# Kernel optimization log

Hardware: AMD Instinct MI355X
Metric: run time of the kernel (lower is better)

## Reference

```python
import jax, jax.numpy as jnp
import numpy as np

WS = 800      # window size
HEADS = 3
DH = 24       # dim_head
LOWRANK_W = 30
NEG_SLOPE = 0.01  # LeakyReLU default
LN_EPS = 1e-5


def _layernorm(x, g, b):
    m = jnp.mean(x, axis=-1, keepdims=True)
    v = jnp.var(x, axis=-1, keepdims=True)
    return (x - m) * jax.lax.rsqrt(v + LN_EPS) * g + b


def setup_inputs() -> dict:
    key = jax.random.key(0)
    ks = jax.random.split(key, 20)
    B, CIN, H, W = 2, 5, 160, 160
    D = 48
    INNER = HEADS * DH  # 72
    f32 = jnp.float32

    def n(k, shape, s=0.05):
        return jax.random.normal(k, shape, f32) * s

    return {
        "x": jax.random.normal(ks[0], (B, CIN, H, W), f32),
        # Embedding: Conv2d(5, 48, 3, pad=1) + PReLU
        "conv_w": n(ks[1], (D, CIN, 3, 3), 0.1),
        "conv_b": jnp.zeros((D,), f32),
        "prelu_a": jnp.array(0.25, f32),
        # attention PreNorm
        "ln1_g": jnp.ones((D,), f32),
        "ln1_b": jnp.zeros((D,), f32),
        # to_qkv: Linear(48, 216, bias=False)
        "w_qkv": n(ks[2], (3 * INNER, D)),
        # Linformer low-rank params E,F: [heads, dim_head, w]
        "E_mat": jax.random.normal(ks[3], (HEADS, DH, LOWRANK_W), f32),
        "F_mat": jax.random.normal(ks[4], (HEADS, DH, LOWRANK_W), f32),
        # lin1/lin2: Linear(w, dim_head)
        "w_e": n(ks[5], (DH, LOWRANK_W)),
        "b_e": jnp.zeros((DH,), f32),
        "w_f": n(ks[6], (DH, LOWRANK_W)),
        "b_f": jnp.zeros((DH,), f32),
        # to_out: Linear(72, 48)
        "w_out": n(ks[7], (D, INNER)),
        "b_out": jnp.zeros((D,), f32),
        # FF PreNorm + MLP (dim=48, hidden=48)
        "ln2_g": jnp.ones((D,), f32),
        "ln2_b": jnp.zeros((D,), f32),
        "ff_w1": n(ks[8], (D, D)),
        "ff_b1": jnp.zeros((D,), f32),
        "ff_w2": n(ks[9], (D, D)),
        "ff_b2": jnp.zeros((D,), f32),
        # final lin1: Linear(48, 96)
        "w_fin": n(ks[10], (2 * D, D)),
        "b_fin": jnp.zeros((2 * D,), f32),
    }


def reference(x, conv_w, conv_b, prelu_a, ln1_g, ln1_b, w_qkv, E_mat, F_mat,
              w_e, b_e, w_f, b_f, w_out, b_out, ln2_g, ln2_b,
              ff_w1, ff_b1, ff_w2, ff_b2, w_fin, b_fin):
    B, _, H, W = x.shape
    # Embedding: conv3x3 same + PReLU
    E = jax.lax.conv_general_dilated(
        x, conv_w, (1, 1), ((1, 1), (1, 1)),
        dimension_numbers=("NCHW", "OIHW", "NCHW")) + conv_b[None, :, None, None]
    E = jnp.maximum(E, 0) + prelu_a * jnp.minimum(E, 0)
    D = E.shape[1]
    seq = E.reshape(B, D, H * W).transpose(0, 2, 1)  # [B, N, D]
    N = seq.shape[1]
    nw = N // WS

    # --- Residual(PreNorm(LinformerAttention_wind1)) ---
    xn = _layernorm(seq, ln1_g, ln1_b)
    xw = xn.reshape(B, nw, WS, D)                         # windows
    qkv = jnp.einsum("bwnc,oc->bwno", xw, w_qkv)          # [B,nw,WS,216]
    qkv = qkv.reshape(B, nw, WS, HEADS, 3 * DH).transpose(0, 1, 3, 2, 4)
    q, k, v = jnp.split(qkv, 3, axis=-1)                  # each [B,nw,h,WS,DH]
    # einsum 'b h n d, h d d -> b h n d' == scale by diagonal of lin(E/F)
    e_diag = jnp.einsum("hdw,dw->hd", E_mat, w_e) + b_e   # [h, DH]
    f_diag = jnp.einsum("hdw,dw->hd", F_mat, w_f) + b_f
    k = k * e_diag[None, None, :, None, :]
    v = v * f_diag[None, None, :, None, :]
    scale = DH ** -0.5
    dots = jnp.einsum("bwhid,bwhjd->bwhij", q, k) * scale  # [B,nw,h,WS,WS]
    attn = jax.nn.softmax(dots, axis=-1)
    ow = jnp.einsum("bwhij,bwhjd->bwhid", attn, v)
    ow = ow.transpose(0, 1, 3, 2, 4).reshape(B, N, HEADS * DH)
    att = jnp.einsum("bnf,of->bno", ow, w_out) + b_out
    seq = seq + att

    # --- Residual(PreNorm(FeedForward)) ---
    yn = _layernorm(seq, ln2_g, ln2_b)
    h = jnp.einsum("bnc,oc->bno", yn, ff_w1) + ff_b1
    h = jnp.where(h >= 0, h, NEG_SLOPE * h)
    h = jnp.einsum("bno,co->bnc", h, ff_w2) + ff_b2
    att1 = seq + h                                        # [B, N, D]

    hp = att1.transpose(0, 2, 1).reshape(B, D, H, W)
    Highpass1 = E * hp + E
    lin = jnp.einsum("bnc,oc->bno", att1, w_fin) + b_fin  # [B, N, 2D]
    return (Highpass1, lin)
```

## Files before the change

kernel.cpp:

```cpp
#include <hip/hip_runtime.h>
#include <hip/hip_bf16.h>

#define B_    2
#define CIN_  5
#define H_    160
#define W_    160
#define N_    25600
#define D_    48
#define NW_   32
#define WS_   800
#define HEADS_ 3
#define DH_   24
#define INNER_ 72
#define NWH_  192

typedef __bf16 bf16x8 __attribute__((ext_vector_type(8)));
typedef float  f32x4  __attribute__((ext_vector_type(4)));

#define MFMA(a,b,c) __builtin_amdgcn_mfma_f32_16x16x32_bf16((a),(b),(c),0,0,0)

__device__ __forceinline__ float fast_exp2(float x) {
#if __has_builtin(__builtin_amdgcn_exp2f)
    return __builtin_amdgcn_exp2f(x);
#else
    return exp2f(x);
#endif
}

__device__ __forceinline__ unsigned pack_bf16(float lo, float hi) {
    __bf16 l = (__bf16)lo, h = (__bf16)hi;
    unsigned short ul = __builtin_bit_cast(unsigned short, l);
    unsigned short uh = __builtin_bit_cast(unsigned short, h);
    return ((unsigned)uh << 16) | (unsigned)ul;
}

__global__ __launch_bounds__(256) void k_wprep(const float* __restrict__ wqkv,
                                               const float* __restrict__ w_out,
                                               const float* __restrict__ fw1,
                                               const float* __restrict__ fw2,
                                               const float* __restrict__ wfin,
                                               const float* __restrict__ cw,
                                               const float* __restrict__ Em,
                                               const float* __restrict__ Fm,
                                               const float* __restrict__ we,
                                               const float* __restrict__ be,
                                               const float* __restrict__ wf,
                                               const float* __restrict__ bf,
                                               float* __restrict__ diag,
                                               __bf16* __restrict__ wqB,
                                               __bf16* __restrict__ woB,
                                               __bf16* __restrict__ f1B,
                                               __bf16* __restrict__ f2B,
                                               __bf16* __restrict__ wfB,
                                               __bf16* __restrict__ wcB) {
    if (blockIdx.x == 0 && threadIdx.x < 72) {
        int tt = threadIdx.x;
        int h = tt / 24, d = tt % 24;
        float se = be[d], sf = bf[d];
        for (int w = 0; w < 30; ++w) {
            se += Em[(h*24+d)*30 + w] * we[d*30 + w];
            sf += Fm[(h*24+d)*30 + w] * wf[d*30 + w];
        }
        diag[tt]      = se;
        diag[72 + tt] = sf;
    }
    int t = blockIdx.x*256 + threadIdx.x, stride = gridDim.x*256;
    for (int i = t; i < 288*64; i += stride) {
        int grow = i>>6, c = i&63;
        int gg = grow>>5, q = grow&31, tt = q>>4, sp = q&15, d = tt*16+sp;
        int part = gg/3, head = gg%3;
        wqB[i] = (d<24 && c<48) ? (__bf16)wqkv[(head*72 + part*24 + d)*48 + c] : (__bf16)0.f;
    }
    for (int i = t; i < 48*96;  i += stride) {
        int o = i/96, p = i%96;
        int h = p>>5, q = p&31, j = q&1, sp = q>>1, d = j*16+sp;
        woB[i] = (d<24) ? (__bf16)w_out[o*72 + h*24 + d] : (__bf16)0.f;
    }
    for (int i = t; i < 48*64;  i += stride) { int o=i>>6, c=i&63; f1B[i] = (c<48)? (__bf16)fw1[o*48+c] : (__bf16)0.f; }
    for (int i = t; i < 48*64;  i += stride) { int o=i>>6, c=i&63; f2B[i] = (c<48)? (__bf16)fw2[o*48+c] : (__bf16)0.f; }
    for (int i = t; i < 96*64;  i += stride) { int o=i>>6, c=i&63; wfB[i] = (c<48)? (__bf16)wfin[o*48+c] : (__bf16)0.f; }
    for (int i = t; i < 48*64;  i += stride) { int o=i>>6, c=i&63; wcB[i] = (c<45)? (__bf16)cw[o*45+c] : (__bf16)0.f; }
}

__global__ __launch_bounds__(128) void k_cqkv(const float* __restrict__ x,
                                              const __bf16* __restrict__ wcB,
                                              const float* __restrict__ cb,
                                              const float* __restrict__ pa,
                                              const __bf16* __restrict__ wqB,
                                              const float* __restrict__ g1,
                                              const float* __restrict__ b1,
                                              const float* __restrict__ diag,
                                              float* __restrict__ seqT,
                                              __bf16* __restrict__ Qbf,
                                              __bf16* __restrict__ Kbf,
                                              __bf16* __restrict__ Vt) {
    __shared__ float Lx[CIN_][4][W_];
    __shared__ __bf16 ic2[64*64];
    __shared__ __bf16 xfer[2][2048];
    int t = threadIdx.x;
    int blk = blockIdx.x;
    int b = blk / 400;
    int n0 = (blk % 400) * 64;
    int y0 = n0 / W_;

    for (int i = t; i < CIN_*4*W_; i += 128) {
        int ic = i / (4*W_), rem = i % (4*W_), yy = rem / W_, col = rem % W_;
        int yr = y0 - 1 + yy;
        float v = 0.f;
        if (yr >= 0 && yr < H_)
            v = x[((size_t)(b*CIN_ + ic)*H_ + yr)*W_ + col];
        Lx[ic][yy][col] = v;
    }
    __syncthreads();

    {
        int px = t & 63;
        int hf = t >> 6;
        int n  = n0 + px;
        int y  = n / W_, xx = n % W_;
        int dy = y - y0;
        char* ib = (char*)ic2;
        int sw = (px&7) << 4;
        if (hf == 0) {
            #pragma unroll
            for (int k = 0; k < 32; ++k) {
                int ic = k/9, rem = k%9, ky = rem/3, kx = rem%3;
                int xc = xx + kx - 1;
                float v = (xc >= 0 && xc < W_) ? Lx[ic][dy+ky][xc] : 0.f;
                *(__bf16*)(ib + ((px*128 + k*2) ^ sw)) = (__bf16)v;
            }
        } else {
            #pragma unroll
            for (int j = 0; j < 32; ++j) {
                int k = 32 + j;
                float v = 0.f;
                if (k < 45) {
                    int ic = k/9, rem = k%9, ky = rem/3, kx = rem%3;
                    int xc = xx + kx - 1;
                    v = (xc >= 0 && xc < W_) ? Lx[ic][dy+ky][xc] : 0.f;
                }
                *(__bf16*)(ib + ((px*128 + k*2) ^ sw)) = (__bf16)v;
            }
        }
    }
    __syncthreads();

    int wv = t >> 6, lane = t & 63, g = lane>>4, s = lane&15;
    int grow0 = blk*64 + wv*32;

    bf16x8 ac[2][2];
    {
        char* ib = (char*)ic2;
        #pragma unroll
        for (int m = 0; m < 2; ++m)
          #pragma unroll
          for (int kc = 0; kc < 2; ++kc) {
            int row = wv*32 + m*16 + s;
            ac[m][kc] = *(const bf16x8*)(ib + ((row*128 + kc*64 + g*16) ^ ((row&7)<<4)));
          }
    }
    const bf16x8* WC4 = (const bf16x8*)wcB;
    float a = pa[0];
    float cbv[3];
    #pragma unroll
    for (int n = 0; n < 3; ++n) cbv[n] = cb[n*16+s];

    float xr[2][3][4];
    #pragma unroll
    for (int n = 0; n < 3; ++n) {
        bf16x8 wb0 = WC4[(n*16+s)*8 + g];
        bf16x8 wb1 = WC4[(n*16+s)*8 + 4 + g];
        #pragma unroll
        for (int m = 0; m < 2; ++m) {
            f32x4 c = {0.f,0.f,0.f,0.f};
            c = MFMA(ac[m][0], wb0, c);
            c = MFMA(ac[m][1], wb1, c);
            #pragma unroll
            for (int r = 0; r < 4; ++r) {
                float vv = c[r] + cbv[n];
                vv = vv >= 0.f ? vv : a * vv;
                xr[m][n][r] = vv;
            }
        }
    }
    #pragma unroll
    for (int m = 0; m < 2; ++m)
      #pragma unroll
      for (int n = 0; n < 3; ++n)
        #pragma unroll
        for (int r = 0; r < 4; ++r)
          seqT[(size_t)(grow0 + m*16 + g*4 + r)*48 + n*16 + s] = xr[m][n][r];

    char* xb = (char*)&xfer[wv][0];
    int nrem = grow0 % N_;
    int w = nrem / WS_, i0 = nrem % WS_;
    size_t headbase = (size_t)((b*NW_ + w)*HEADS_);

    float g1v[3], b1v[3];
    #pragma unroll
    for (int n = 0; n < 3; ++n) { g1v[n] = g1[n*16+s]; b1v[n] = b1[n*16+s]; }

    #pragma unroll
    for (int m = 0; m < 2; ++m)
      #pragma unroll
      for (int r = 0; r < 4; ++r) {
        float sm = xr[m][0][r] + xr[m][1][r] + xr[m][2][r];
        float sq = xr[m][0][r]*xr[m][0][r] + xr[m][1][r]*xr[m][1][r] + xr[m][2][r]*xr[m][2][r];
        #pragma unroll
        for (int msk = 1; msk < 16; msk <<= 1) { sm += __shfl_xor(sm, msk); sq += __shfl_xor(sq, msk); }
        float mean = sm * (1.f/48.f);
        float var  = sq * (1.f/48.f) - mean*mean;
        float rs   = rsqrtf(var + 1e-5f);
        int row = m*16 + g*4 + r;
        int sw  = ((g*4+r)&7) << 4;
        #pragma unroll
        for (int n = 0; n < 3; ++n) {
            float yn = (xr[m][n][r] - mean) * rs * g1v[n] + b1v[n];
            *(__bf16*)(xb + ((row*128 + (n*16+s)*2) ^ sw)) = (__bf16)yn;
        }
        *(__bf16*)(xb + ((row*128 + (48+s)*2) ^ sw)) = (__bf16)0.f;
      }

    bf16x8 af[2][2];
    #pragma unroll
    for (int m = 0; m < 2; ++m)
      #pragma unroll
      for (int kc = 0; kc < 2; ++kc)
        af[m][kc] = *(const bf16x8*)(xb + (((m*16+s)*128 + kc*64 + g*16) ^ ((s&7)<<4)));

    const bf16x8* WQ4 = (const bf16x8*)wqB;
    const float SCALE = 0.2944889919f;

    float dke[3], dko[3], dve[3], dvo[3];
    #pragma unroll
    for (int h = 0; h < 3; ++h) {
        dke[h] = diag[h*24 + s];
        dko[h] = (s < 8) ? diag[h*24 + 16 + s] : 0.f;
        dve[h] = diag[72 + h*24 + s];
        dvo[h] = (s < 8) ? diag[72 + h*24 + 16 + s] : 0.f;
    }

    unsigned* Qd = (unsigned*)Qbf;
    unsigned* Kd = (unsigned*)Kbf;

    #pragma unroll
    for (int gg = 0; gg < 9; ++gg) {
        int part = gg / 3, head = gg % 3;
        bf16x8 we0 = WQ4[(gg*32 +      s)*8 +     g];
        bf16x8 we1 = WQ4[(gg*32 +      s)*8 + 4 + g];
        bf16x8 wo0 = WQ4[(gg*32 + 16 + s)*8 +     g];
        bf16x8 wo1 = WQ4[(gg*32 + 16 + s)*8 + 4 + g];
        f32x4 ce[2], co[2];
        #pragma unroll
        for (int m = 0; m < 2; ++m) {
            f32x4 c = {0.f,0.f,0.f,0.f};
            c = MFMA(af[m][0], we0, c); c = MFMA(af[m][1], we1, c);
            ce[m] = c;
            f32x4 d = {0.f,0.f,0.f,0.f};
            d = MFMA(af[m][0], wo0, d); d = MFMA(af[m][1], wo1, d);
            co[m] = d;
        }
        size_t rbase = (headbase + head)*WS_ + i0;
        if (part == 0) {
            #pragma unroll
            for (int m = 0; m < 2; ++m)
              #pragma unroll
              for (int r = 0; r < 4; ++r)
                Qd[(rbase + m*16 + g*4 + r)*16 + s] =
                    pack_bf16(ce[m][r]*SCALE, co[m][r]*SCALE);
        } else if (part == 1) {
            #pragma unroll
            for (int m = 0; m < 2; ++m)
              #pragma unroll
              for (int r = 0; r < 4; ++r) {
                int p5 = 16*(g&1) + 8*m + 4*(g>>1) + r;
                Kd[(rbase + p5)*16 + s] =
                    pack_bf16(ce[m][r]*dke[head], co[m][r]*dko[head]);
              }
        } else {
            size_t vbase = (headbase + head)*((size_t)32*WS_) + i0;
            #pragma unroll
            for (int m = 0; m < 2; ++m)
              #pragma unroll
              for (int r = 0; r < 4; ++r) {
                int row = m*16 + g*4 + r;
                Vt[vbase + (size_t)s*WS_ + row] = (__bf16)(ce[m][r]*dve[head]);
                if (s < 8)
                    Vt[vbase + (size_t)(16+s)*WS_ + row] = (__bf16)(co[m][r]*dvo[head]);
              }
        }
    }
    unsigned* Vd = (unsigned*)Vt;
    #pragma unroll
    for (int it = 0; it < 6; ++it) {
        int idx = it*64 + lane;
        int h = idx >> 7, rem = idx & 127;
        int dd = 24 + (rem >> 4), cp = rem & 15;
        size_t ubase = (((headbase + h)*((size_t)32*WS_) + (size_t)dd*WS_ + i0) >> 1);
        Vd[ubase + cp] = (dd == 24) ? 0x3F803F80u : 0u;
    }
}

__global__ __launch_bounds__(256, 4) void k_attn(const __bf16* __restrict__ Qbf,
                                                 const __bf16* __restrict__ Kbf,
                                                 const __bf16* __restrict__ Vt,
                                                 __bf16* __restrict__ OW) {
    __shared__ float red[2][5][2][4][64];
    int t = threadIdx.x;
    int wv = t >> 6, lane = t & 63;
    int g = lane >> 4, s = lane & 15;
    int half = wv & 1, tsk = wv >> 1;
    int blk = blockIdx.x;
    int v = (blk & 7) * 120 + (blk >> 3);
    int task = v * 2 + tsk;
    int wh = task / 10, qt = task % 10;
    int q0 = qt * 80;

    const bf16x8* Qp = (const bf16x8*)(Qbf + ((size_t)wh*WS_ + q0)*32);
    const bf16x8* Kp = (const bf16x8*)(Kbf + (size_t)wh*WS_*32);
    const bf16x8* Vp = (const bf16x8*)(Vt  + (size_t)wh*32*WS_);

    bf16x8 qb[5];
    #pragma unroll
    for (int i = 0; i < 5; ++i) qb[i] = Qp[(i*16 + s)*4 + g];

    f32x4 o[5][2];
    #pragma unroll
    for (int i = 0; i < 5; ++i) {
        o[i][0] = (f32x4){0.f,0.f,0.f,0.f};
        o[i][1] = (f32x4){0.f,0.f,0.f,0.f};
    }

    int c0 = half ? 12 : 0;
    int c1 = half ? 25 : 12;

    bf16x8 ka0 = Kp[(c0*32 + s)*4 + g];
    bf16x8 ka1 = Kp[(c0*32 + 16 + s)*4 + g];
    bf16x8 vb0 = Vp[s*100 + c0*4 + g];
    bf16x8 vb1 = Vp[(16+s)*100 + c0*4 + g];

    for (int c = c0; c < c1; ++c) {
        int cn = (c + 1 < c1) ? c + 1 : c0;
        bf16x8 nk0 = Kp[(cn*32 + s)*4 + g];
        bf16x8 nk1 = Kp[(cn*32 + 16 + s)*4 + g];
        bf16x8 nv0 = Vp[s*100 + cn*4 + g];
        bf16x8 nv1 = Vp[(16+s)*100 + cn*4 + g];

        #pragma unroll
        for (int i = 0; i < 5; ++i) {
            f32x4 s0 = {0.f,0.f,0.f,0.f}, s1 = {0.f,0.f,0.f,0.f};
            s0 = MFMA(ka0, qb[i], s0);
            s1 = MFMA(ka1, qb[i], s1);
            bf16x8 pa;
            #pragma unroll
            for (int r = 0; r < 4; ++r) {
                pa[r]     = (__bf16)fast_exp2(s0[r]);
                pa[r + 4] = (__bf16)fast_exp2(s1[r]);
            }
            o[i][0] = MFMA(pa, vb0, o[i][0]);
            o[i][1] = MFMA(pa, vb1, o[i][1]);
        }
        ka0 = nk0; ka1 = nk1; vb0 = nv0; vb1 = nv1;
    }

    if (half) {
        #pragma unroll
        for (int i = 0; i < 5; ++i)
          #pragma unroll
          for (int j = 0; j < 2; ++j)
            #pragma unroll
            for (int r = 0; r < 4; ++r)
              red[tsk][i][j][r][lane] = o[i][j][r];
    }
    __syncthreads();
    if (!half) {
        #pragma unroll
        for (int i = 0; i < 5; ++i)
          #pragma unroll
          for (int j = 0; j < 2; ++j)
            #pragma unroll
            for (int r = 0; r < 4; ++r)
              o[i][j][r] += red[tsk][i][j][r][lane];

        int bw = wh / 3, h = wh % 3;
        int b = bw >> 5, w = bw & 31;
        unsigned* OWd = (unsigned*)OW;
        #pragma unroll
        for (int i = 0; i < 5; ++i) {
            #pragma unroll
            for (int r = 0; r < 4; ++r) {
                float den = __shfl(o[i][1][r], (lane & 48) + 8);
                float inv = 1.f / den;
                int n = w*WS_ + q0 + i*16 + g*4 + r;
                OWd[(size_t)(b*N_ + n)*48 + h*16 + s] =
                    pack_bf16(o[i][0][r]*inv, o[i][1][r]*inv);
            }
        }
    }
}

__global__ __launch_bounds__(256) void k_tail(const float* __restrict__ seqT,
                                              const __bf16* __restrict__ OW,
                                              const __bf16* __restrict__ woB,
                                              const float* __restrict__ b_out,
                                              const float* __restrict__ g2,
                                              const float* __restrict__ b2,
                                              const __bf16* __restrict__ f1B,
                                              const float* __restrict__ fb1,
                                              const __bf16* __restrict__ f2B,
                                              const float* __restrict__ fb2,
                                              const __bf16* __restrict__ wfB,
                                              const float* __restrict__ bfin,
                                              float* __restrict__ out1,
                                              float* __restrict__ out2) {
    __shared__ __bf16 xfer[4][2048];
    __shared__ float hp[4][32][49];
    int t = threadIdx.x, wv = t>>6, lane = t&63, g = lane>>4, s = lane&15;
    int row0 = (blockIdx.x*4 + wv) * 32;
    char* xb = (char*)&xfer[wv][0];

    int b = row0 / N_;
    int nbase = row0 % N_;

    const bf16x8* OW4 = (const bf16x8*)OW;
    const bf16x8* WO4 = (const bf16x8*)woB;
    const bf16x8* F14 = (const bf16x8*)f1B;
    const bf16x8* F24 = (const bf16x8*)f2B;
    const bf16x8* WF4 = (const bf16x8*)wfB;

    bf16x8 aow[2][3];
    #pragma unroll
    for (int m = 0; m < 2; ++m)
      #pragma unroll
      for (int kc = 0; kc < 3; ++kc)
        aow[m][kc] = OW4[(size_t)(row0 + m*16 + s)*12 + kc*4 + g];

    f32x4 s2[2][3];
    #pragma unroll
    for (int n = 0; n < 3; ++n) {
        bf16x8 wb0 = WO4[(n*16+s)*12 + g];
        bf16x8 wb1 = WO4[(n*16+s)*12 + 4 + g];
        bf16x8 wb2 = WO4[(n*16+s)*12 + 8 + g];
        #pragma unroll
        for (int m = 0; m < 2; ++m) {
            f32x4 c = {0.f,0.f,0.f,0.f};
            c = MFMA(aow[m][0], wb0, c);
            c = MFMA(aow[m][1], wb1, c);
            c = MFMA(aow[m][2], wb2, c);
            s2[m][n] = c;
        }
    }
    float bov[3], g2v[3], b2v[3], f1bv[3], f2bv[3];
    #pragma unroll
    for (int n = 0; n < 3; ++n) {
        bov[n] = b_out[n*16+s]; g2v[n] = g2[n*16+s]; b2v[n] = b2[n*16+s];
        f1bv[n] = fb1[n*16+s];  f2bv[n] = fb2[n*16+s];
    }
    float sv[2][3][4];
    #pragma unroll
    for (int m = 0; m < 2; ++m)
      #pragma unroll
      for (int n = 0; n < 3; ++n)
        #pragma unroll
        for (int r = 0; r < 4; ++r) {
          sv[m][n][r] = seqT[(size_t)(row0 + m*16 + g*4 + r)*48 + n*16 + s];
          s2[m][n][r] += sv[m][n][r] + bov[n];
        }

    #pragma unroll
    for (int m = 0; m < 2; ++m)
      #pragma unroll
      for (int r = 0; r < 4; ++r) {
        float sm = s2[m][0][r] + s2[m][1][r] + s2[m][2][r];
        float sq = s2[m][0][r]*s2[m][0][r] + s2[m][1][r]*s2[m][1][r] + s2[m][2][r]*s2[m][2][r];
        #pragma unroll
        for (int msk = 1; msk < 16; msk <<= 1) { sm += __shfl_xor(sm, msk); sq += __shfl_xor(sq, msk); }
        float mean = sm * (1.f/48.f);
        float var  = sq * (1.f/48.f) - mean*mean;
        float rs   = rsqrtf(var + 1e-5f);
        int row = m*16 + g*4 + r;
        int sw  = ((g*4+r)&7) << 4;
        #pragma unroll
        for (int n = 0; n < 3; ++n) {
            float yn = (s2[m][n][r] - mean) * rs * g2v[n] + b2v[n];
            *(__bf16*)(xb + ((row*128 + (n*16+s)*2) ^ sw)) = (__bf16)yn;
        }
        *(__bf16*)(xb + ((row*128 + (48+s)*2) ^ sw)) = (__bf16)0.f;
      }

    bf16x8 af[2][2];
    f32x4 hh[2][3];

    #pragma unroll
    for (int m = 0; m < 2; ++m)
      #pragma unroll
      for (int kc = 0; kc < 2; ++kc)
        af[m][kc] = *(const bf16x8*)(xb + (((m*16+s)*128 + kc*64 + g*16) ^ ((s&7)<<4)));
    #pragma unroll
    for (int n = 0; n < 3; ++n) {
        bf16x8 wb0 = F14[(n*16+s)*8 + g];
        bf16x8 wb1 = F14[(n*16+s)*8 + 4 + g];
        #pragma unroll
        for (int m = 0; m < 2; ++m) {
            f32x4 c = {0.f,0.f,0.f,0.f};
            c = MFMA(af[m][0], wb0, c);
            c = MFMA(af[m][1], wb1, c);
            hh[m][n] = c;
        }
    }
    #pragma unroll
    for (int m = 0; m < 2; ++m)
      #pragma unroll
      for (int r = 0; r < 4; ++r) {
        int row = m*16 + g*4 + r;
        int sw  = ((g*4+r)&7) << 4;
        #pragma unroll
        for (int n = 0; n < 3; ++n) {
            float v = hh[m][n][r] + f1bv[n];
            v = v >= 0.f ? v : 0.01f*v;
            *(__bf16*)(xb + ((row*128 + (n*16+s)*2) ^ sw)) = (__bf16)v;
        }
        *(__bf16*)(xb + ((row*128 + (48+s)*2) ^ sw)) = (__bf16)0.f;
      }

    #pragma unroll
    for (int m = 0; m < 2; ++m)
      #pragma unroll
      for (int kc = 0; kc < 2; ++kc)
        af[m][kc] = *(const bf16x8*)(xb + (((m*16+s)*128 + kc*64 + g*16) ^ ((s&7)<<4)));
    #pragma unroll
    for (int n = 0; n < 3; ++n) {
        bf16x8 wb0 = F24[(n*16+s)*8 + g];
        bf16x8 wb1 = F24[(n*16+s)*8 + 4 + g];
        #pragma unroll
        for (int m = 0; m < 2; ++m) {
            f32x4 c = {0.f,0.f,0.f,0.f};
            c = MFMA(af[m][0], wb0, c);
            c = MFMA(af[m][1], wb1, c);
            hh[m][n] = c;
        }
    }
    #pragma unroll
    for (int m = 0; m < 2; ++m)
      #pragma unroll
      for (int r = 0; r < 4; ++r) {
        int row = m*16 + g*4 + r;
        int sw  = ((g*4+r)&7) << 4;
        #pragma unroll
        for (int n = 0; n < 3; ++n) {
            float a1v = s2[m][n][r] + hh[m][n][r] + f2bv[n];
            hp[wv][row][n*16+s] = sv[m][n][r] * (1.f + a1v);
            *(__bf16*)(xb + ((row*128 + (n*16+s)*2) ^ sw)) = (__bf16)a1v;
        }
        *(__bf16*)(xb + ((row*128 + (48+s)*2) ^ sw)) = (__bf16)0.f;
      }

    #pragma unroll
    for (int it = 0; it < 6; ++it) {
        int flat = it*256 + lane*4;
        int ch = flat >> 5, row = flat & 31;
        float4 v = { hp[wv][row][ch], hp[wv][row+1][ch],
                     hp[wv][row+2][ch], hp[wv][row+3][ch] };
        *(float4*)&out1[((size_t)b*D_ + ch)*N_ + nbase + row] = v;
    }

    #pragma unroll
    for (int m = 0; m < 2; ++m)
      #pragma unroll
      for (int kc = 0; kc < 2; ++kc)
        af[m][kc] = *(const bf16x8*)(xb + (((m*16+s)*128 + kc*64 + g*16) ^ ((s&7)<<4)));
    #pragma unroll
    for (int n = 0; n < 6; ++n) {
        bf16x8 wb0 = WF4[(n*16+s)*8 + g];
        bf16x8 wb1 = WF4[(n*16+s)*8 + 4 + g];
        float bfv = bfin[n*16+s];
        #pragma unroll
        for (int m = 0; m < 2; ++m) {
            f32x4 c = {0.f,0.f,0.f,0.f};
            c = MFMA(af[m][0], wb0, c);
            c = MFMA(af[m][1], wb1, c);
            #pragma unroll
            for (int r = 0; r < 4; ++r)
                out2[(size_t)(row0 + m*16 + g*4 + r)*96 + n*16 + s] = c[r] + bfv;
        }
    }
}

extern "C" void kernel_launch(void* const* d_in, const int* in_sizes, int n_in,
                              void* d_out, int out_size, void* d_ws, size_t ws_size,
                              hipStream_t stream) {
    const float* x      = (const float*)d_in[0];
    const float* conv_w = (const float*)d_in[1];
    const float* conv_b = (const float*)d_in[2];
    const float* prelu_a= (const float*)d_in[3];
    const float* ln1_g  = (const float*)d_in[4];
    const float* ln1_b  = (const float*)d_in[5];
    const float* w_qkv  = (const float*)d_in[6];
    const float* E_mat  = (const float*)d_in[7];
    const float* F_mat  = (const float*)d_in[8];
    const float* w_e    = (const float*)d_in[9];
    const float* b_e    = (const float*)d_in[10];
    const float* w_f    = (const float*)d_in[11];
    const float* b_f    = (const float*)d_in[12];
    const float* w_out  = (const float*)d_in[13];
    const float* b_out  = (const float*)d_in[14];
    const float* ln2_g  = (const float*)d_in[15];
    const float* ln2_b  = (const float*)d_in[16];
    const float* ff_w1  = (const float*)d_in[17];
    const float* ff_b1  = (const float*)d_in[18];
    const float* ff_w2  = (const float*)d_in[19];
    const float* ff_b2  = (const float*)d_in[20];
    const float* w_fin  = (const float*)d_in[21];
    const float* b_fin  = (const float*)d_in[22];

    float* ws = (float*)d_ws;
    float*  seqT = ws;
    float*  diag = seqT + (size_t)B_*N_*D_;
    __bf16* Qbf  = (__bf16*)(diag + 144);
    __bf16* Kbf  = Qbf + (size_t)NWH_*WS_*32;
    __bf16* Vt   = Kbf + (size_t)NWH_*WS_*32;
    __bf16* OW   = Vt + (size_t)NWH_*32*WS_;
    __bf16* wqB  = OW + (size_t)B_*N_*96;
    __bf16* woB  = wqB + 288*64;
    __bf16* f1B  = woB + 48*96;
    __bf16* f2B  = f1B + 48*64;
    __bf16* wfB  = f2B + 48*64;
    __bf16* wcB  = wfB + 96*64;

    float* out1 = (float*)d_out;
    float* out2 = out1 + (size_t)B_*D_*N_;

    k_wprep<<<32, 256, 0, stream>>>(w_qkv, w_out, ff_w1, ff_w2, w_fin, conv_w,
                                    E_mat, F_mat, w_e, b_e, w_f, b_f, diag,
                                    wqB, woB, f1B, f2B, wfB, wcB);
    k_cqkv<<<800, 128, 0, stream>>>(x, wcB, conv_b, prelu_a,
                                    wqB, ln1_g, ln1_b, diag, seqT, Qbf, Kbf, Vt);
    k_attn<<<960, 256, 0, stream>>>(Qbf, Kbf, Vt, OW);
    k_tail<<<400, 256, 0, stream>>>(seqT, OW, woB, b_out, ln2_g, ln2_b,
                                    f1B, ff_b1, f2B, ff_b2, wfB, b_fin,
                                    out1, out2);
}
```

Before: 81.58 us.

## Give each wave a full-key-range 32-query tile, dropping split-K LDS reduction

Result: slower. 88.55 us (+8.5%).

```diff
diff --git a/kernel.cpp b/kernel.cpp
--- a/kernel.cpp
+++ b/kernel.cpp
@@ -305,49 +305,44 @@
                                                  const __bf16* __restrict__ Kbf,
                                                  const __bf16* __restrict__ Vt,
                                                  __bf16* __restrict__ OW) {
-    __shared__ float red[2][5][2][4][64];
     int t = threadIdx.x;
     int wv = t >> 6, lane = t & 63;
     int g = lane >> 4, s = lane & 15;
-    int half = wv & 1, tsk = wv >> 1;
     int blk = blockIdx.x;
-    int v = (blk & 7) * 120 + (blk >> 3);
-    int task = v * 2 + tsk;
-    int wh = task / 10, qt = task % 10;
-    int q0 = qt * 80;
+    int v = (blk & 7) * 150 + (blk >> 3);
+    int task = v * 4 + wv;
+    int wh = task / 25, qt = task % 25;
+    int q0 = qt * 32;
 
     const bf16x8* Qp = (const bf16x8*)(Qbf + ((size_t)wh*WS_ + q0)*32);
     const bf16x8* Kp = (const bf16x8*)(Kbf + (size_t)wh*WS_*32);
     const bf16x8* Vp = (const bf16x8*)(Vt  + (size_t)wh*32*WS_);
 
-    bf16x8 qb[5];
-    #pragma unroll
-    for (int i = 0; i < 5; ++i) qb[i] = Qp[(i*16 + s)*4 + g];
-
-    f32x4 o[5][2];
-    #pragma unroll
-    for (int i = 0; i < 5; ++i) {
+    bf16x8 qb[2];
+    #pragma unroll
+    for (int i = 0; i < 2; ++i) qb[i] = Qp[(i*16 + s)*4 + g];
+
+    f32x4 o[2][2];
+    #pragma unroll
+    for (int i = 0; i < 2; ++i) {
         o[i][0] = (f32x4){0.f,0.f,0.f,0.f};
         o[i][1] = (f32x4){0.f,0.f,0.f,0.f};
     }
 
-    int c0 = half ? 12 : 0;
-    int c1 = half ? 25 : 12;
-
-    bf16x8 ka0 = Kp[(c0*32 + s)*4 + g];
-    bf16x8 ka1 = Kp[(c0*32 + 16 + s)*4 + g];
-    bf16x8 vb0 = Vp[s*100 + c0*4 + g];
-    bf16x8 vb1 = Vp[(16+s)*100 + c0*4 + g];
-
-    for (int c = c0; c < c1; ++c) {
-        int cn = (c + 1 < c1) ? c + 1 : c0;
+    bf16x8 ka0 = Kp[s*4 + g];
+    bf16x8 ka1 = Kp[(16 + s)*4 + g];
+    bf16x8 vb0 = Vp[s*100 + g];
+    bf16x8 vb1 = Vp[(16+s)*100 + g];
+
+    for (int c = 0; c < 25; ++c) {
+        int cn = (c + 1 < 25) ? c + 1 : 0;
         bf16x8 nk0 = Kp[(cn*32 + s)*4 + g];
         bf16x8 nk1 = Kp[(cn*32 + 16 + s)*4 + g];
         bf16x8 nv0 = Vp[s*100 + cn*4 + g];
         bf16x8 nv1 = Vp[(16+s)*100 + cn*4 + g];
 
         #pragma unroll
-        for (int i = 0; i < 5; ++i) {
+        for (int i = 0; i < 2; ++i) {
             f32x4 s0 = {0.f,0.f,0.f,0.f}, s1 = {0.f,0.f,0.f,0.f};
             s0 = MFMA(ka0, qb[i], s0);
             s1 = MFMA(ka1, qb[i], s1);
@@ -363,38 +358,18 @@
         ka0 = nk0; ka1 = nk1; vb0 = nv0; vb1 = nv1;
     }
 
-    if (half) {
-        #pragma unroll
-        for (int i = 0; i < 5; ++i)
-          #pragma unroll
-          for (int j = 0; j < 2; ++j)
-            #pragma unroll
-            for (int r = 0; r < 4; ++r)
-              red[tsk][i][j][r][lane] = o[i][j][r];
-    }
-    __syncthreads();
-    if (!half) {
-        #pragma unroll
-        for (int i = 0; i < 5; ++i)
-          #pragma unroll
-          for (int j = 0; j < 2; ++j)
-            #pragma unroll
-            for (int r = 0; r < 4; ++r)
-              o[i][j][r] += red[tsk][i][j][r][lane];
-
-        int bw = wh / 3, h = wh % 3;
-        int b = bw >> 5, w = bw & 31;
-        unsigned* OWd = (unsigned*)OW;
-        #pragma unroll
-        for (int i = 0; i < 5; ++i) {
-            #pragma unroll
-            for (int r = 0; r < 4; ++r) {
-                float den = __shfl(o[i][1][r], (lane & 48) + 8);
-                float inv = 1.f / den;
-                int n = w*WS_ + q0 + i*16 + g*4 + r;
-                OWd[(size_t)(b*N_ + n)*48 + h*16 + s] =
-                    pack_bf16(o[i][0][r]*inv, o[i][1][r]*inv);
-            }
+    int bw = wh / 3, h = wh % 3;
+    int b = bw >> 5, w = bw & 31;
+    unsigned* OWd = (unsigned*)OW;
+    #pragma unroll
+    for (int i = 0; i < 2; ++i) {
+        #pragma unroll
+        for (int r = 0; r < 4; ++r) {
+            float den = __shfl(o[i][1][r], (lane & 48) + 8);
+            float inv = 1.f / den;
+            int n = w*WS_ + q0 + i*16 + g*4 + r;
+            OWd[(size_t)(b*N_ + n)*48 + h*16 + s] =
+                pack_bf16(o[i][0][r]*inv, o[i][1][r]*inv);
         }
     }
 }
@@ -635,7 +610,7 @@
                                     wqB, woB, f1B, f2B, wfB, wcB);
     k_cqkv<<<800, 128, 0, stream>>>(x, wcB, conv_b, prelu_a,
                                     wqB, ln1_g, ln1_b, diag, seqT, Qbf, Kbf, Vt);
-    k_attn<<<960, 256, 0, stream>>>(Qbf, Kbf, Vt, OW);
+    k_attn<<<1200, 256, 0, stream>>>(Qbf, Kbf, Vt, OW);
     k_tail<<<400, 256, 0, stream>>>(seqT, OW, woB, b_out, ln2_g, ln2_b,
                                     f1B, ff_b1, f2B, ff_b2, wfB, b_fin,
                                     out1, out2);
```
